# Kernel optimization log

Measured on AMD Instinct MI355X. Metric: run time of the kernel, lower is better.

Reference implementation:

```python
import jax, jax.numpy as jnp
import numpy as np

N = 50000      # nodes
E = 800000     # edges
D = 128        # input_dim
HID = 128      # hidden_dim
OUT = 128      # output_dim
NH = 16        # n_heads (head_dim = 8)
EF = 16        # edge_feat_dim
RF = 64        # r_feat_dim
KV = 2 * D + EF + RF  # 336


def _ln(x, g, b):
    m = x.mean(-1, keepdims=True)
    v = ((x - m) ** 2).mean(-1, keepdims=True)
    return (x - m) / jnp.sqrt(v + 1e-5) * g + b


def _mlp(x, W1, b1, g, be, W2, b2):
    # Linear -> LayerNorm -> ReLU -> Linear (targetdiff-style MLP, norm=True)
    h = jax.nn.relu(_ln(x @ W1 + b1, g, be))
    return h @ W2 + b2


def setup_inputs() -> dict:
    key = jax.random.key(0)
    ks = jax.random.split(key, 32)

    def w(k, shape, fan_in):
        return (jax.random.normal(k, shape, jnp.float32) / np.sqrt(fan_in)).astype(jnp.float32)

    inp = {
        'h': jax.random.normal(ks[0], (N, D), jnp.float32),
        'rel_x': jax.random.normal(ks[1], (E, 3), jnp.float32),
        'r_feat': jax.random.normal(ks[2], (E, RF), jnp.float32),
        'edge_feat': jax.random.normal(ks[3], (E, EF), jnp.float32),
        'edge_index': jax.random.randint(ks[4], (2, E), 0, N, jnp.int64 if jax.config.jax_enable_x64 else jnp.int32),
        # xk MLP: KV -> HID -> OUT
        'xk_W1': w(ks[5], (KV, HID), KV), 'xk_b1': jnp.zeros((HID,), jnp.float32),
        'xk_g': jnp.ones((HID,), jnp.float32), 'xk_be': jnp.zeros((HID,), jnp.float32),
        'xk_W2': w(ks[6], (HID, OUT), HID), 'xk_b2': jnp.zeros((OUT,), jnp.float32),
        # xv MLP: KV -> HID -> NH
        'xv_W1': w(ks[7], (KV, HID), KV), 'xv_b1': jnp.zeros((HID,), jnp.float32),
        'xv_g': jnp.ones((HID,), jnp.float32), 'xv_be': jnp.zeros((HID,), jnp.float32),
        'xv_W2': w(ks[8], (HID, NH), HID), 'xv_b2': jnp.zeros((NH,), jnp.float32),
        # xq MLP: D -> HID -> OUT
        'xq_W1': w(ks[9], (D, HID), D), 'xq_b1': jnp.zeros((HID,), jnp.float32),
        'xq_g': jnp.ones((HID,), jnp.float32), 'xq_be': jnp.zeros((HID,), jnp.float32),
        'xq_W2': w(ks[10], (HID, OUT), HID), 'xq_b2': jnp.zeros((OUT,), jnp.float32),
        # edge-weight net: Linear(RF,1) + sigmoid
        'ew_W': w(ks[11], (RF, 1), RF), 'ew_b': jnp.zeros((1,), jnp.float32),
    }
    return inp


def reference(h, rel_x, r_feat, edge_feat, edge_index,
              xk_W1, xk_b1, xk_g, xk_be, xk_W2, xk_b2,
              xv_W1, xv_b1, xv_g, xv_be, xv_W2, xv_b2,
              xq_W1, xq_b1, xq_g, xq_be, xq_W2, xq_b2,
              ew_W, ew_b):
    src, dst = edge_index[0], edge_index[1]
    # gather -> MLPs
    kv_input = jnp.concatenate([edge_feat, r_feat, h[dst], h[src]], axis=-1)  # [E, KV]
    k = _mlp(kv_input, xk_W1, xk_b1, xk_g, xk_be, xk_W2, xk_b2).reshape(-1, NH, OUT // NH)
    v = _mlp(kv_input, xv_W1, xv_b1, xv_g, xv_be, xv_W2, xv_b2)              # [E, NH]
    e_w = jax.nn.sigmoid(r_feat @ ew_W + ew_b)                               # [E, 1]
    v = v * e_w
    v = v[:, :, None] * rel_x[:, None, :]                                    # [E, NH, 3]
    q = _mlp(h, xq_W1, xq_b1, xq_g, xq_be, xq_W2, xq_b2).reshape(-1, NH, OUT // NH)
    # scatter-softmax over dst segments
    s = (q[dst] * k).sum(-1) / np.sqrt(OUT // NH)                            # [E, NH]
    smax = jax.ops.segment_max(s, dst, num_segments=N)
    ex = jnp.exp(s - smax[dst])
    den = jax.ops.segment_sum(ex, dst, num_segments=N)
    alpha = ex / den[dst]                                                     # [E, NH]
    m = alpha[:, :, None] * v                                                 # [E, NH, 3]
    out = jax.ops.segment_sum(m, dst, num_segments=N)                         # [N, NH, 3]
    return out.mean(1)                                                        # [N, 3]
```

## Files before the change

kernel.cpp:

```cpp
#include <hip/hip_runtime.h>
#include <hip/hip_bf16.h>

#define NN 50000
#define NE 800000
#define DD 128
#define NHD 16
#define EFD 16
#define RFD 64
#define KVD 336
#define KST 360
#define ME 64
#define HST 136
#define KSS 132

typedef __attribute__((ext_vector_type(8))) short bf16x8;
typedef __attribute__((ext_vector_type(4))) float f32x4;

__device__ __forceinline__ unsigned short f2bf(float f) {
    __hip_bfloat16 h = __float2bfloat16(f);
    return __builtin_bit_cast(unsigned short, h);
}
__device__ __forceinline__ float bf2f(unsigned short u) {
    return __uint_as_float(((unsigned)u) << 16);
}

__global__ __launch_bounds__(256) void prep_wt(
    const float* __restrict__ xkW1, const float* __restrict__ xvW1,
    unsigned short* __restrict__ Wt)
{
    const int n = blockIdx.x;
    const float* W = (n < 128) ? xkW1 : xvW1;
    const int col = n & 127;
    for (int k = threadIdx.x; k < KST; k += 256) {
        float v = (k < KVD) ? W[(size_t)k * 128 + col] : 0.0f;
        Wt[(size_t)n * KST + k] = f2bf(v);
    }
}

__global__ __launch_bounds__(128) void prep_wt2(
    const float* __restrict__ xkW2, const float* __restrict__ xvW2,
    unsigned short* __restrict__ Wt2)
{
    const int n = blockIdx.x;
    const int k = threadIdx.x;
    float v = (n < 128) ? xkW2[(size_t)k * 128 + n]
                        : xvW2[(size_t)k * 16 + (n - 128)];
    Wt2[(size_t)n * 128 + k] = f2bf(v);
}

__global__ __launch_bounds__(256) void prep_hbf(
    const float* __restrict__ h, unsigned short* __restrict__ hb)
{
    const size_t i = ((size_t)blockIdx.x * 256 + threadIdx.x) * 4;
    const float4 f = *(const float4*)&h[i];
    ushort4 o;
    o.x = f2bf(f.x); o.y = f2bf(f.y); o.z = f2bf(f.z); o.w = f2bf(f.w);
    *(ushort4*)&hb[i] = o;
}

__global__ __launch_bounds__(256) void hist_kernel(
    const int* __restrict__ dst, int* __restrict__ deg)
{
    const int i = blockIdx.x * 256 + threadIdx.x;
    if (i < NE) atomicAdd(&deg[dst[i]], 1);
}

__global__ __launch_bounds__(256) void scan_kernel(
    const int* __restrict__ deg, int* __restrict__ off, int* __restrict__ cur)
{
    __shared__ int wsum[4];
    const int t = threadIdx.x;
    const int lane = t & 63;
    const int w = t >> 6;
    int run = 0;
    for (int base = 0; base < NN; base += 256) {
        int v = (base + t < NN) ? deg[base + t] : 0;
        int x = v;
        #pragma unroll
        for (int o2 = 1; o2 < 64; o2 <<= 1) {
            int y = __shfl_up(x, o2);
            if (lane >= o2) x += y;
        }
        if (lane == 63) wsum[w] = x;
        __syncthreads();
        int pre = 0;
        #pragma unroll
        for (int ww = 0; ww < 4; ww++) if (ww < w) pre += wsum[ww];
        const int tot = wsum[0] + wsum[1] + wsum[2] + wsum[3];
        const int excl = run + pre + x - v;
        if (base + t < NN) { off[base + t] = excl; cur[base + t] = excl; }
        run += tot;
        __syncthreads();
    }
    if (t == 0) off[NN] = run;
}

__global__ __launch_bounds__(256) void scatter_kernel(
    const int* __restrict__ dst, int* __restrict__ cur, int* __restrict__ eidx)
{
    const int i = blockIdx.x * 256 + threadIdx.x;
    if (i < NE) {
        const int p = atomicAdd(&cur[dst[i]], 1);
        eidx[p] = i;
    }
}

__global__ __launch_bounds__(128) void qmlp_kernel(
    const float* __restrict__ h,
    const float* __restrict__ W1, const float* __restrict__ b1,
    const float* __restrict__ g,  const float* __restrict__ be,
    const float* __restrict__ W2, const float* __restrict__ b2,
    unsigned short* __restrict__ q_bf)
{
    __shared__ float hs[4][DD];
    __shared__ float hid[4][DD];
    __shared__ float red[4][2][2];
    const int j  = threadIdx.x;
    const int n0 = blockIdx.x * 4;

    #pragma unroll
    for (int n = 0; n < 4; n++) hs[n][j] = h[(size_t)(n0 + n) * DD + j];
    __syncthreads();

    float a[4];
    #pragma unroll
    for (int n = 0; n < 4; n++) a[n] = b1[j];
    #pragma unroll 8
    for (int i = 0; i < DD; i++) {
        float w = W1[i * DD + j];
        #pragma unroll
        for (int n = 0; n < 4; n++) a[n] = fmaf(hs[n][i], w, a[n]);
    }

    const int wid = j >> 6;
    #pragma unroll
    for (int n = 0; n < 4; n++) {
        float s1 = a[n], s2 = a[n] * a[n];
        #pragma unroll
        for (int off = 32; off > 0; off >>= 1) {
            s1 += __shfl_xor(s1, off);
            s2 += __shfl_xor(s2, off);
        }
        if ((j & 63) == 0) { red[n][0][wid] = s1; red[n][1][wid] = s2; }
    }
    __syncthreads();

    const float gg = g[j], bb = be[j];
    #pragma unroll
    for (int n = 0; n < 4; n++) {
        float s1   = red[n][0][0] + red[n][0][1];
        float s2   = red[n][1][0] + red[n][1][1];
        float mean = s1 * (1.0f / DD);
        float var  = s2 * (1.0f / DD) - mean * mean;
        float r    = (a[n] - mean) * rsqrtf(var + 1e-5f) * gg + bb;
        hid[n][j]  = fmaxf(r, 0.0f);
    }
    __syncthreads();

    float o[4];
    #pragma unroll
    for (int n = 0; n < 4; n++) o[n] = b2[j];
    #pragma unroll 8
    for (int i = 0; i < DD; i++) {
        float w = W2[i * DD + j];
        #pragma unroll
        for (int n = 0; n < 4; n++) o[n] = fmaf(hid[n][i], w, o[n]);
    }
    #pragma unroll
    for (int n = 0; n < 4; n++) q_bf[(size_t)(n0 + n) * DD + j] = f2bf(o[n]);
}

union SharedU {
    unsigned short kv[ME * KST];
    struct {
        unsigned short hidk[ME * HST];
        unsigned short hidv[ME * HST];
    } s2;
    float ks[ME * KSS];
};

template<int MODE>
__global__ __launch_bounds__(256, 3) void edge_kernel(
    const unsigned short* __restrict__ h_bf,
    const float* __restrict__ rel_x,
    const float* __restrict__ r_feat,
    const float* __restrict__ edge_feat,
    const int*   __restrict__ e_src,
    const int*   __restrict__ e_dst,
    const unsigned short* __restrict__ Wt,
    const unsigned short* __restrict__ Wt2,
    const float* __restrict__ xk_b1, const float* __restrict__ xk_g,
    const float* __restrict__ xk_be, const float* __restrict__ xk_b2,
    const float* __restrict__ xv_b1, const float* __restrict__ xv_g,
    const float* __restrict__ xv_be, const float* __restrict__ xv_W2,
    const float* __restrict__ xv_b2,
    const float* __restrict__ ew_W,  const float* __restrict__ ew_b,
    const unsigned short* __restrict__ q_bf,
    float* __restrict__ exv,
    float* __restrict__ vwe,
    float* __restrict__ accN)
{
    __shared__ SharedU u;
    __shared__ float v_s[ME][NHD + 1];
    __shared__ float ew_s[ME];
    __shared__ float rel_s[ME][3];
    __shared__ int   dst_s[ME];
    __shared__ int   src_s[ME];

    const int tid = threadIdx.x;
    const int e0  = blockIdx.x * ME;

    if (tid < ME) { dst_s[tid] = e_dst[e0 + tid]; src_s[tid] = e_src[e0 + tid]; }
    else if (MODE == 0) {
        int t = tid - ME;
        rel_s[t / 3][t % 3] = rel_x[(size_t)e0 * 3 + t];
    }
    __syncthreads();

    {
        const int e = tid >> 2, p = tid & 3;
        const size_t ge = (size_t)(e0 + e);
        {
            float4 f = *(const float4*)&edge_feat[ge * EFD + p * 4];
            ushort4 o; o.x = f2bf(f.x); o.y = f2bf(f.y); o.z = f2bf(f.z); o.w = f2bf(f.w);
            *(ushort4*)&u.kv[e * KST + p * 4] = o;
        }
        {
            float part = 0.0f;
            #pragma unroll
            for (int i = 0; i < 4; i++) {
                float4 f = *(const float4*)&r_feat[ge * RFD + p * 16 + i * 4];
                float4 w = *(const float4*)&ew_W[p * 16 + i * 4];
                part += f.x * w.x + f.y * w.y + f.z * w.z + f.w * w.w;
                ushort4 o; o.x = f2bf(f.x); o.y = f2bf(f.y); o.z = f2bf(f.z); o.w = f2bf(f.w);
                *(ushort4*)&u.kv[e * KST + 16 + p * 16 + i * 4] = o;
            }
            part += __shfl_xor(part, 1);
            part += __shfl_xor(part, 2);
            if (p == 0) ew_s[e] = 1.0f / (1.0f + __expf(-(part + ew_b[0])));
        }
        {
            const uint4* hp = (const uint4*)&h_bf[(size_t)dst_s[e] * DD + p * 32];
            uint4* op = (uint4*)&u.kv[e * KST + 80 + p * 32];
            #pragma unroll
            for (int i = 0; i < 4; i++) op[i] = hp[i];
        }
        {
            const uint4* hp = (const uint4*)&h_bf[(size_t)src_s[e] * DD + p * 32];
            uint4* op = (uint4*)&u.kv[e * KST + 208 + p * 32];
            #pragma unroll
            for (int i = 0; i < 4; i++) op[i] = hp[i];
        }
        if (p < 2) {
            uint4 z = make_uint4(0, 0, 0, 0);
            *(uint4*)&u.kv[e * KST + 336 + p * 8] = z;
        }
    }
    __syncthreads();

    const int lane = tid & 63;
    const int wv   = tid >> 6;
    const int half = wv >> 1;
    const int mrow = (wv & 1) * 32;
    const int c15  = lane & 15;
    const int q    = lane >> 4;

    f32x4 acc[2][8];
    #pragma unroll
    for (int mt = 0; mt < 2; mt++)
        #pragma unroll
        for (int nt = 0; nt < 8; nt++) acc[mt][nt] = (f32x4){0.f, 0.f, 0.f, 0.f};

    {
        const unsigned short* WtH = Wt + (size_t)(half * 128 + c15) * KST;
        const unsigned short* kvA = &u.kv[(mrow + c15) * KST];
        for (int ks = 0; ks < 11; ks++) {
            const int k0 = ks * 32 + q * 8;
            bf16x8 a0 = *(const bf16x8*)&kvA[k0];
            bf16x8 a1 = *(const bf16x8*)&kvA[16 * KST + k0];
            #pragma unroll
            for (int nt = 0; nt < 8; nt++) {
                bf16x8 b = *(const bf16x8*)&WtH[(size_t)nt * 16 * KST + k0];
                acc[0][nt] = __builtin_amdgcn_mfma_f32_16x16x32_bf16(a0, b, acc[0][nt], 0, 0, 0);
                acc[1][nt] = __builtin_amdgcn_mfma_f32_16x16x32_bf16(a1, b, acc[1][nt], 0, 0, 0);
            }
        }
    }

    {
        const float* b1p = half ? xv_b1 : xk_b1;
        const float* gp  = half ? xv_g  : xk_g;
        const float* bep = half ? xv_be : xk_be;
        float bia[8], gam[8], bet[8];
        #pragma unroll
        for (int nt = 0; nt < 8; nt++) {
            int idx = nt * 16 + c15;
            bia[nt] = b1p[idx]; gam[nt] = gp[idx]; bet[nt] = bep[idx];
        }
        #pragma unroll
        for (int mt = 0; mt < 2; mt++)
            #pragma unroll
            for (int r = 0; r < 4; r++) {
                float x[8]; float s1 = 0.f, s2 = 0.f;
                #pragma unroll
                for (int nt = 0; nt < 8; nt++) {
                    x[nt] = acc[mt][nt][r] + bia[nt];
                    s1 += x[nt]; s2 = fmaf(x[nt], x[nt], s2);
                }
                #pragma unroll
                for (int off = 1; off < 16; off <<= 1) {
                    s1 += __shfl_xor(s1, off);
                    s2 += __shfl_xor(s2, off);
                }
                float mean = s1 * (1.0f / 128.0f);
                float var  = s2 * (1.0f / 128.0f) - mean * mean;
                float rstd = rsqrtf(var + 1e-5f);
                #pragma unroll
                for (int nt = 0; nt < 8; nt++)
                    acc[mt][nt][r] = fmaxf((x[nt] - mean) * rstd * gam[nt] + bet[nt], 0.0f);
            }
    }
    __syncthreads();

    {
        unsigned short* hdst = half ? u.s2.hidv : u.s2.hidk;
        #pragma unroll
        for (int mt = 0; mt < 2; mt++)
            #pragma unroll
            for (int r = 0; r < 4; r++) {
                const int row = mrow + mt * 16 + q * 4 + r;
                #pragma unroll
                for (int nt = 0; nt < 8; nt++)
                    hdst[row * HST + nt * 16 + c15] = f2bf(acc[mt][nt][r]);
            }
    }
    __syncthreads();

    const int mb2 = (wv & 1) * 32;
    const int nb2 = (wv >> 1) * 64;
    f32x4 acck[2][4];
    #pragma unroll
    for (int mt = 0; mt < 2; mt++)
        #pragma unroll
        for (int nt = 0; nt < 4; nt++) acck[mt][nt] = (f32x4){0.f, 0.f, 0.f, 0.f};
    {
        const unsigned short* A0 = &u.s2.hidk[(mb2 + c15) * HST];
        const unsigned short* A1 = &u.s2.hidk[(mb2 + 16 + c15) * HST];
        const unsigned short* B0 = &Wt2[(size_t)(nb2 + c15) * 128];
        #pragma unroll
        for (int ks = 0; ks < 4; ks++) {
            const int k0 = ks * 32 + q * 8;
            bf16x8 a0 = *(const bf16x8*)&A0[k0];
            bf16x8 a1 = *(const bf16x8*)&A1[k0];
            #pragma unroll
            for (int nt = 0; nt < 4; nt++) {
                bf16x8 b = *(const bf16x8*)&B0[(size_t)nt * 16 * 128 + k0];
                acck[0][nt] = __builtin_amdgcn_mfma_f32_16x16x32_bf16(a0, b, acck[0][nt], 0, 0, 0);
                acck[1][nt] = __builtin_amdgcn_mfma_f32_16x16x32_bf16(a1, b, acck[1][nt], 0, 0, 0);
            }
        }
    }

    float vacc[4];
    #pragma unroll
    for (int p = 0; p < 4; p++) {
        int item = tid + p * 256;
        int e    = item >> 4;
        int col  = item & 15;
        float a = xv_b2[col];
        #pragma unroll 8
        for (int i4 = 0; i4 < 32; i4++) {
            const ushort4 hv = *(const ushort4*)&u.s2.hidv[e * HST + i4 * 4];
            a = fmaf(bf2f(hv.x), xv_W2[(i4 * 4 + 0) * 16 + col], a);
            a = fmaf(bf2f(hv.y), xv_W2[(i4 * 4 + 1) * 16 + col], a);
            a = fmaf(bf2f(hv.z), xv_W2[(i4 * 4 + 2) * 16 + col], a);
            a = fmaf(bf2f(hv.w), xv_W2[(i4 * 4 + 3) * 16 + col], a);
        }
        vacc[p] = a;
    }
    __syncthreads();

    #pragma unroll
    for (int nt = 0; nt < 4; nt++) {
        const float bias = xk_b2[nb2 + nt * 16 + c15];
        #pragma unroll
        for (int mt = 0; mt < 2; mt++)
            #pragma unroll
            for (int r = 0; r < 4; r++)
                u.ks[(mb2 + mt * 16 + q * 4 + r) * KSS + nb2 + nt * 16 + c15] =
                    acck[mt][nt][r] + bias;
    }
    #pragma unroll
    for (int p = 0; p < 4; p++) {
        int item = tid + p * 256;
        v_s[item >> 4][item & 15] = vacc[p];
    }
    __syncthreads();

    {
        const float inv_s8 = 0.35355339059327373f;
        const int tc2  = tid & 31;
        const int te2  = tid >> 5;
        const int head = tc2 >> 1;
        const int sub  = tc2 & 1;
        #pragma unroll
        for (int e = 0; e < 8; e++) {
            int el  = te2 * 8 + e;
            int dst = dst_s[el];
            const float4  kk = *(const float4*)&u.ks[el * KSS + tc2 * 4];
            const ushort4 qb = *(const ushort4*)&q_bf[(size_t)dst * DD + tc2 * 4];
            float p = bf2f(qb.x) * kk.x + bf2f(qb.y) * kk.y +
                      bf2f(qb.z) * kk.z + bf2f(qb.w) * kk.w;
            p += __shfl_xor(p, 1);
            float ex = __expf(p * inv_s8);
            if (MODE == 1) {
                if (sub == 0) {
                    exv[(size_t)(e0 + el) * NHD + head] = ex;
                } else {
                    vwe[(size_t)(e0 + el) * NHD + head] =
                        v_s[el][head] * ew_s[el] * ex;
                }
            } else {
                float vw = v_s[el][head] * ew_s[el] * ex;
                float* base = &accN[(((size_t)dst * NHD) + head) * 4];
                if (sub == 0) {
                    atomicAdd(base + 0, vw * rel_s[el][0]);
                    atomicAdd(base + 1, vw * rel_s[el][1]);
                } else {
                    atomicAdd(base + 2, vw * rel_s[el][2]);
                    atomicAdd(base + 3, ex);
                }
            }
        }
    }
}

__global__ __launch_bounds__(256) void gather_kernel(
    const int* __restrict__ off, const int* __restrict__ eidx,
    const float* __restrict__ exv, const float* __restrict__ vwe,
    const float* __restrict__ rel_x, float* __restrict__ out)
{
    const int t = threadIdx.x;
    const int g = t >> 4;
    const int h = t & 15;
    const int n = blockIdx.x * 16 + g;
    if (n >= NN) return;
    const int j0 = off[n], j1 = off[n + 1];
    float den = 0.f, sx = 0.f, sy = 0.f, sz = 0.f;
    for (int j = j0; j < j1; j++) {
        const int e = eidx[j];
        const float ex = exv[(size_t)e * NHD + h];
        const float vw = vwe[(size_t)e * NHD + h];
        const float rx = rel_x[(size_t)e * 3 + 0];
        const float ry = rel_x[(size_t)e * 3 + 1];
        const float rz = rel_x[(size_t)e * 3 + 2];
        sx = fmaf(vw, rx, sx);
        sy = fmaf(vw, ry, sy);
        sz = fmaf(vw, rz, sz);
        den += ex;
    }
    const float c = (den > 0.f) ? 1.0f / den : 0.0f;
    float ox = sx * c, oy = sy * c, oz = sz * c;
    #pragma unroll
    for (int o2 = 1; o2 < 16; o2 <<= 1) {
        ox += __shfl_xor(ox, o2);
        oy += __shfl_xor(oy, o2);
        oz += __shfl_xor(oz, o2);
    }
    if (h == 0) {
        out[(size_t)n * 3 + 0] = ox * (1.0f / NHD);
        out[(size_t)n * 3 + 1] = oy * (1.0f / NHD);
        out[(size_t)n * 3 + 2] = oz * (1.0f / NHD);
    }
}

__global__ __launch_bounds__(256) void finalize_kernel(
    const float* __restrict__ accN, float* __restrict__ out)
{
    int n = blockIdx.x * blockDim.x + threadIdx.x;
    if (n >= NN) return;
    float ox = 0.0f, oy = 0.0f, oz = 0.0f;
    #pragma unroll
    for (int hh = 0; hh < NHD; hh++) {
        float4 a = *(const float4*)&accN[(((size_t)n * NHD) + hh) * 4];
        if (a.w > 0.0f) {
            float r = 1.0f / a.w;
            ox = fmaf(a.x, r, ox);
            oy = fmaf(a.y, r, oy);
            oz = fmaf(a.z, r, oz);
        }
    }
    out[n * 3 + 0] = ox * (1.0f / NHD);
    out[n * 3 + 1] = oy * (1.0f / NHD);
    out[n * 3 + 2] = oz * (1.0f / NHD);
}

extern "C" void kernel_launch(void* const* d_in, const int* in_sizes, int n_in,
                              void* d_out, int out_size, void* d_ws, size_t ws_size,
                              hipStream_t stream)
{
    const float* h         = (const float*)d_in[0];
    const float* rel_x     = (const float*)d_in[1];
    const float* r_feat    = (const float*)d_in[2];
    const float* edge_feat = (const float*)d_in[3];
    const int*   e_idx     = (const int*)d_in[4];
    const float* xk_W1 = (const float*)d_in[5];
    const float* xk_b1 = (const float*)d_in[6];
    const float* xk_g  = (const float*)d_in[7];
    const float* xk_be = (const float*)d_in[8];
    const float* xk_W2 = (const float*)d_in[9];
    const float* xk_b2 = (const float*)d_in[10];
    const float* xv_W1 = (const float*)d_in[11];
    const float* xv_b1 = (const float*)d_in[12];
    const float* xv_g  = (const float*)d_in[13];
    const float* xv_be = (const float*)d_in[14];
    const float* xv_W2 = (const float*)d_in[15];
    const float* xv_b2 = (const float*)d_in[16];
    const float* xq_W1 = (const float*)d_in[17];
    const float* xq_b1 = (const float*)d_in[18];
    const float* xq_g  = (const float*)d_in[19];
    const float* xq_be = (const float*)d_in[20];
    const float* xq_W2 = (const float*)d_in[21];
    const float* xq_b2 = (const float*)d_in[22];
    const float* ew_W  = (const float*)d_in[23];
    const float* ew_b  = (const float*)d_in[24];

    size_t o = 0;
    auto take = [&](size_t bytes) -> char* {
        o = (o + 255) & ~(size_t)255;
        char* p = (char*)d_ws + o;
        o += bytes;
        return p;
    };
    unsigned short* h_bf = (unsigned short*)take((size_t)NN * DD * 2);
    unsigned short* q_bf = (unsigned short*)take((size_t)NN * DD * 2);
    unsigned short* Wt   = (unsigned short*)take((size_t)256 * KST * 2);
    unsigned short* Wt2  = (unsigned short*)take((size_t)144 * 128 * 2);
    int*   deg  = (int*)take((size_t)NN * 4);
    int*   cur  = (int*)take((size_t)NN * 4);
    int*   offv = (int*)take((size_t)(NN + 1) * 4);
    int*   eidx = (int*)take((size_t)NE * 4);
    float* exv  = (float*)take((size_t)NE * NHD * 4);
    float* vwe  = (float*)take((size_t)NE * NHD * 4);
    const bool sorted = (o <= ws_size);
    float* accN = (float*)(void*)deg;

    prep_hbf<<<(NN * DD / 4 + 255) / 256, 256, 0, stream>>>(h, h_bf);
    prep_wt<<<256, 256, 0, stream>>>(xk_W1, xv_W1, Wt);
    prep_wt2<<<144, 128, 0, stream>>>(xk_W2, xv_W2, Wt2);
    qmlp_kernel<<<NN / 4, 128, 0, stream>>>(h, xq_W1, xq_b1, xq_g, xq_be,
                                            xq_W2, xq_b2, q_bf);

    if (sorted) {
        hipMemsetAsync(deg, 0, (size_t)NN * 4, stream);
        hist_kernel<<<(NE + 255) / 256, 256, 0, stream>>>(e_idx + NE, deg);
        scan_kernel<<<1, 256, 0, stream>>>(deg, offv, cur);
        scatter_kernel<<<(NE + 255) / 256, 256, 0, stream>>>(e_idx + NE, cur, eidx);

        edge_kernel<1><<<NE / ME, 256, 0, stream>>>(
            h_bf, rel_x, r_feat, edge_feat,
            e_idx, e_idx + NE,
            Wt, Wt2,
            xk_b1, xk_g, xk_be, xk_b2,
            xv_b1, xv_g, xv_be, xv_W2, xv_b2,
            ew_W, ew_b, q_bf, exv, vwe, nullptr);

        gather_kernel<<<(NN + 15) / 16, 256, 0, stream>>>(
            offv, eidx, exv, vwe, rel_x, (float*)d_out);
    } else {
        hipMemsetAsync(accN, 0, (size_t)NN * NHD * 4 * sizeof(float), stream);
        edge_kernel<0><<<NE / ME, 256, 0, stream>>>(
            h_bf, rel_x, r_feat, edge_feat,
            e_idx, e_idx + NE,
            Wt, Wt2,
            xk_b1, xk_g, xk_be, xk_b2,
            xv_b1, xv_g, xv_be, xv_W2, xv_b2,
            ew_W, ew_b, q_bf, nullptr, nullptr, accN);

        finalize_kernel<<<(NN + 255) / 256, 256, 0, stream>>>(accN, (float*)d_out);
    }
}
```

Before: 1.415 ms.

## Write edge outputs in dst-sorted order, halve edge tile, widen q-MLP blocks

The scatter kernel now records each edge's sorted position and copies rel_x into sorted order. The edge kernel writes exv/vwe straight to those positions, so the gather reads contiguous memory instead of going through eidx indirection. The edge tile drops from 64 to 32 edges per block with a higher occupancy hint, which halves accumulator registers per wave but reuses weight loads less. The q-MLP now handles 16 nodes per 256-thread block to reuse weights better.

```diff
diff --git a/kernel.cpp b/kernel.cpp
--- a/kernel.cpp
+++ b/kernel.cpp
@@ -9,7 +9,7 @@
 #define RFD 64
 #define KVD 336
 #define KST 360
-#define ME 64
+#define ME 32
 #define HST 136
 #define KSS 132
 
@@ -96,78 +96,89 @@
 }
 
 __global__ __launch_bounds__(256) void scatter_kernel(
-    const int* __restrict__ dst, int* __restrict__ cur, int* __restrict__ eidx)
+    const int* __restrict__ dst, const float* __restrict__ rel_x,
+    int* __restrict__ cur, int* __restrict__ pos, float* __restrict__ relp)
 {
     const int i = blockIdx.x * 256 + threadIdx.x;
     if (i < NE) {
         const int p = atomicAdd(&cur[dst[i]], 1);
-        eidx[p] = i;
-    }
-}
-
-__global__ __launch_bounds__(128) void qmlp_kernel(
+        pos[i] = p;
+        relp[(size_t)p * 3 + 0] = rel_x[(size_t)i * 3 + 0];
+        relp[(size_t)p * 3 + 1] = rel_x[(size_t)i * 3 + 1];
+        relp[(size_t)p * 3 + 2] = rel_x[(size_t)i * 3 + 2];
+    }
+}
+
+__global__ __launch_bounds__(256) void qmlp_kernel(
     const float* __restrict__ h,
     const float* __restrict__ W1, const float* __restrict__ b1,
     const float* __restrict__ g,  const float* __restrict__ be,
     const float* __restrict__ W2, const float* __restrict__ b2,
     unsigned short* __restrict__ q_bf)
 {
-    __shared__ float hs[4][DD];
-    __shared__ float hid[4][DD];
-    __shared__ float red[4][2][2];
-    const int j  = threadIdx.x;
-    const int n0 = blockIdx.x * 4;
-
-    #pragma unroll
-    for (int n = 0; n < 4; n++) hs[n][j] = h[(size_t)(n0 + n) * DD + j];
-    __syncthreads();
-
-    float a[4];
-    #pragma unroll
-    for (int n = 0; n < 4; n++) a[n] = b1[j];
+    __shared__ float hs[16][DD];
+    __shared__ float hid[16][DD];
+    __shared__ float red[2][8][2][2];
+    const int tid  = threadIdx.x;
+    const int col  = tid & 127;
+    const int half = tid >> 7;
+    const int wp   = (tid >> 6) & 1;
+    const int n0   = blockIdx.x * 16;
+
+    {
+        const float4* src = (const float4*)&h[(size_t)n0 * DD];
+        float4* dstp = (float4*)&hs[0][0];
+        dstp[tid]       = src[tid];
+        dstp[tid + 256] = src[tid + 256];
+    }
+    __syncthreads();
+
+    float a[8];
+    #pragma unroll
+    for (int j = 0; j < 8; j++) a[j] = b1[col];
     #pragma unroll 8
     for (int i = 0; i < DD; i++) {
-        float w = W1[i * DD + j];
-        #pragma unroll
-        for (int n = 0; n < 4; n++) a[n] = fmaf(hs[n][i], w, a[n]);
-    }
-
-    const int wid = j >> 6;
-    #pragma unroll
-    for (int n = 0; n < 4; n++) {
-        float s1 = a[n], s2 = a[n] * a[n];
+        float w = W1[i * DD + col];
+        #pragma unroll
+        for (int j = 0; j < 8; j++) a[j] = fmaf(hs[half * 8 + j][i], w, a[j]);
+    }
+
+    #pragma unroll
+    for (int j = 0; j < 8; j++) {
+        float s1 = a[j], s2 = a[j] * a[j];
         #pragma unroll
         for (int off = 32; off > 0; off >>= 1) {
             s1 += __shfl_xor(s1, off);
             s2 += __shfl_xor(s2, off);
         }
-        if ((j & 63) == 0) { red[n][0][wid] = s1; red[n][1][wid] = s2; }
-    }
-    __syncthreads();
-
-    const float gg = g[j], bb = be[j];
-    #pragma unroll
-    for (int n = 0; n < 4; n++) {
-        float s1   = red[n][0][0] + red[n][0][1];
-        float s2   = red[n][1][0] + red[n][1][1];
+        if ((tid & 63) == 0) { red[half][j][0][wp] = s1; red[half][j][1][wp] = s2; }
+    }
+    __syncthreads();
+
+    const float gg = g[col], bb = be[col];
+    #pragma unroll
+    for (int j = 0; j < 8; j++) {
+        float s1   = red[half][j][0][0] + red[half][j][0][1];
+        float s2   = red[half][j][1][0] + red[half][j][1][1];
         float mean = s1 * (1.0f / DD);
         float var  = s2 * (1.0f / DD) - mean * mean;
-        float r    = (a[n] - mean) * rsqrtf(var + 1e-5f) * gg + bb;
-        hid[n][j]  = fmaxf(r, 0.0f);
-    }
-    __syncthreads();
-
-    float o[4];
-    #pragma unroll
-    for (int n = 0; n < 4; n++) o[n] = b2[j];
+        float r    = (a[j] - mean) * rsqrtf(var + 1e-5f) * gg + bb;
+        hid[half * 8 + j][col] = fmaxf(r, 0.0f);
+    }
+    __syncthreads();
+
+    float o[8];
+    #pragma unroll
+    for (int j = 0; j < 8; j++) o[j] = b2[col];
     #pragma unroll 8
     for (int i = 0; i < DD; i++) {
-        float w = W2[i * DD + j];
-        #pragma unroll
-        for (int n = 0; n < 4; n++) o[n] = fmaf(hid[n][i], w, o[n]);
-    }
-    #pragma unroll
-    for (int n = 0; n < 4; n++) q_bf[(size_t)(n0 + n) * DD + j] = f2bf(o[n]);
+        float w = W2[i * DD + col];
+        #pragma unroll
+        for (int j = 0; j < 8; j++) o[j] = fmaf(hid[half * 8 + j][i], w, o[j]);
+    }
+    #pragma unroll
+    for (int j = 0; j < 8; j++)
+        q_bf[(size_t)(n0 + half * 8 + j) * DD + col] = f2bf(o[j]);
 }
 
 union SharedU {
@@ -180,13 +191,14 @@
 };
 
 template<int MODE>
-__global__ __launch_bounds__(256, 3) void edge_kernel(
+__global__ __launch_bounds__(256, 6) void edge_kernel(
     const unsigned short* __restrict__ h_bf,
     const float* __restrict__ rel_x,
     const float* __restrict__ r_feat,
     const float* __restrict__ edge_feat,
     const int*   __restrict__ e_src,
     const int*   __restrict__ e_dst,
+    const int*   __restrict__ pos,
     const unsigned short* __restrict__ Wt,
     const unsigned short* __restrict__ Wt2,
     const float* __restrict__ xk_b1, const float* __restrict__ xk_g,
@@ -206,26 +218,25 @@
     __shared__ float rel_s[ME][3];
     __shared__ int   dst_s[ME];
     __shared__ int   src_s[ME];
+    __shared__ int   pos_s[ME];
 
     const int tid = threadIdx.x;
     const int e0  = blockIdx.x * ME;
 
-    if (tid < ME) { dst_s[tid] = e_dst[e0 + tid]; src_s[tid] = e_src[e0 + tid]; }
-    else if (MODE == 0) {
+    if (tid < ME) {
+        dst_s[tid] = e_dst[e0 + tid];
+        src_s[tid] = e_src[e0 + tid];
+        if (MODE == 1) pos_s[tid] = pos[e0 + tid];
+    } else if (MODE == 0 && tid < ME + ME * 3) {
         int t = tid - ME;
         rel_s[t / 3][t % 3] = rel_x[(size_t)e0 * 3 + t];
     }
     __syncthreads();
 
     {
-        const int e = tid >> 2, p = tid & 3;
+        const int e = tid >> 3, p = tid & 7;
         const size_t ge = (size_t)(e0 + e);
-        {
-            float4 f = *(const float4*)&edge_feat[ge * EFD + p * 4];
-            ushort4 o; o.x = f2bf(f.x); o.y = f2bf(f.y); o.z = f2bf(f.z); o.w = f2bf(f.w);
-            *(ushort4*)&u.kv[e * KST + p * 4] = o;
-        }
-        {
+        if (p < 4) {
             float part = 0.0f;
             #pragma unroll
             for (int i = 0; i < 4; i++) {
@@ -238,18 +249,20 @@
             part += __shfl_xor(part, 1);
             part += __shfl_xor(part, 2);
             if (p == 0) ew_s[e] = 1.0f / (1.0f + __expf(-(part + ew_b[0])));
+        } else {
+            float4 f = *(const float4*)&edge_feat[ge * EFD + (p - 4) * 4];
+            ushort4 o; o.x = f2bf(f.x); o.y = f2bf(f.y); o.z = f2bf(f.z); o.w = f2bf(f.w);
+            *(ushort4*)&u.kv[e * KST + (p - 4) * 4] = o;
         }
         {
-            const uint4* hp = (const uint4*)&h_bf[(size_t)dst_s[e] * DD + p * 32];
-            uint4* op = (uint4*)&u.kv[e * KST + 80 + p * 32];
-            #pragma unroll
-            for (int i = 0; i < 4; i++) op[i] = hp[i];
+            const uint4* hp = (const uint4*)&h_bf[(size_t)dst_s[e] * DD + p * 16];
+            uint4* op = (uint4*)&u.kv[e * KST + 80 + p * 16];
+            op[0] = hp[0]; op[1] = hp[1];
         }
         {
-            const uint4* hp = (const uint4*)&h_bf[(size_t)src_s[e] * DD + p * 32];
-            uint4* op = (uint4*)&u.kv[e * KST + 208 + p * 32];
-            #pragma unroll
-            for (int i = 0; i < 4; i++) op[i] = hp[i];
+            const uint4* hp = (const uint4*)&h_bf[(size_t)src_s[e] * DD + p * 16];
+            uint4* op = (uint4*)&u.kv[e * KST + 208 + p * 16];
+            op[0] = hp[0]; op[1] = hp[1];
         }
         if (p < 2) {
             uint4 z = make_uint4(0, 0, 0, 0);
@@ -258,31 +271,27 @@
     }
     __syncthreads();
 
-    const int lane = tid & 63;
-    const int wv   = tid >> 6;
-    const int half = wv >> 1;
-    const int mrow = (wv & 1) * 32;
-    const int c15  = lane & 15;
-    const int q    = lane >> 4;
-
-    f32x4 acc[2][8];
-    #pragma unroll
-    for (int mt = 0; mt < 2; mt++)
-        #pragma unroll
-        for (int nt = 0; nt < 8; nt++) acc[mt][nt] = (f32x4){0.f, 0.f, 0.f, 0.f};
+    const int lane  = tid & 63;
+    const int wv    = tid >> 6;
+    const int half  = wv >> 1;
+    const int mhalf = wv & 1;
+    const int c15   = lane & 15;
+    const int q     = lane >> 4;
+
+    f32x4 acc[8];
+    #pragma unroll
+    for (int nt = 0; nt < 8; nt++) acc[nt] = (f32x4){0.f, 0.f, 0.f, 0.f};
 
     {
         const unsigned short* WtH = Wt + (size_t)(half * 128 + c15) * KST;
-        const unsigned short* kvA = &u.kv[(mrow + c15) * KST];
+        const unsigned short* kvA = &u.kv[(mhalf * 16 + c15) * KST];
         for (int ks = 0; ks < 11; ks++) {
             const int k0 = ks * 32 + q * 8;
             bf16x8 a0 = *(const bf16x8*)&kvA[k0];
-            bf16x8 a1 = *(const bf16x8*)&kvA[16 * KST + k0];
             #pragma unroll
             for (int nt = 0; nt < 8; nt++) {
                 bf16x8 b = *(const bf16x8*)&WtH[(size_t)nt * 16 * KST + k0];
-                acc[0][nt] = __builtin_amdgcn_mfma_f32_16x16x32_bf16(a0, b, acc[0][nt], 0, 0, 0);
-                acc[1][nt] = __builtin_amdgcn_mfma_f32_16x16x32_bf16(a1, b, acc[1][nt], 0, 0, 0);
+                acc[nt] = __builtin_amdgcn_mfma_f32_16x16x32_bf16(a0, b, acc[nt], 0, 0, 0);
             }
         }
     }
@@ -298,72 +307,63 @@
             bia[nt] = b1p[idx]; gam[nt] = gp[idx]; bet[nt] = bep[idx];
         }
         #pragma unroll
-        for (int mt = 0; mt < 2; mt++)
-            #pragma unroll
-            for (int r = 0; r < 4; r++) {
-                float x[8]; float s1 = 0.f, s2 = 0.f;
-                #pragma unroll
-                for (int nt = 0; nt < 8; nt++) {
-                    x[nt] = acc[mt][nt][r] + bia[nt];
-                    s1 += x[nt]; s2 = fmaf(x[nt], x[nt], s2);
-                }
-                #pragma unroll
-                for (int off = 1; off < 16; off <<= 1) {
-                    s1 += __shfl_xor(s1, off);
-                    s2 += __shfl_xor(s2, off);
-                }
-                float mean = s1 * (1.0f / 128.0f);
-                float var  = s2 * (1.0f / 128.0f) - mean * mean;
-                float rstd = rsqrtf(var + 1e-5f);
-                #pragma unroll
-                for (int nt = 0; nt < 8; nt++)
-                    acc[mt][nt][r] = fmaxf((x[nt] - mean) * rstd * gam[nt] + bet[nt], 0.0f);
+        for (int r = 0; r < 4; r++) {
+            float x[8]; float s1 = 0.f, s2 = 0.f;
+            #pragma unroll
+            for (int nt = 0; nt < 8; nt++) {
+                x[nt] = acc[nt][r] + bia[nt];
+                s1 += x[nt]; s2 = fmaf(x[nt], x[nt], s2);
             }
+            #pragma unroll
+            for (int off = 1; off < 16; off <<= 1) {
+                s1 += __shfl_xor(s1, off);
+                s2 += __shfl_xor(s2, off);
+            }
+            float mean = s1 * (1.0f / 128.0f);
+            float var  = s2 * (1.0f / 128.0f) - mean * mean;
+            float rstd = rsqrtf(var + 1e-5f);
+            #pragma unroll
+            for (int nt = 0; nt < 8; nt++)
+                acc[nt][r] = fmaxf((x[nt] - mean) * rstd * gam[nt] + bet[nt], 0.0f);
+        }
     }
     __syncthreads();
 
     {
         unsigned short* hdst = half ? u.s2.hidv : u.s2.hidk;
         #pragma unroll
-        for (int mt = 0; mt < 2; mt++)
-            #pragma unroll
-            for (int r = 0; r < 4; r++) {
-                const int row = mrow + mt * 16 + q * 4 + r;
-                #pragma unroll
-                for (int nt = 0; nt < 8; nt++)
-                    hdst[row * HST + nt * 16 + c15] = f2bf(acc[mt][nt][r]);
-            }
-    }
-    __syncthreads();
-
-    const int mb2 = (wv & 1) * 32;
-    const int nb2 = (wv >> 1) * 64;
-    f32x4 acck[2][4];
-    #pragma unroll
-    for (int mt = 0; mt < 2; mt++)
-        #pragma unroll
-        for (int nt = 0; nt < 4; nt++) acck[mt][nt] = (f32x4){0.f, 0.f, 0.f, 0.f};
+        for (int r = 0; r < 4; r++) {
+            const int row = mhalf * 16 + q * 4 + r;
+            #pragma unroll
+            for (int nt = 0; nt < 8; nt++)
+                hdst[row * HST + nt * 16 + c15] = f2bf(acc[nt][r]);
+        }
+    }
+    __syncthreads();
+
+    const int mb2 = mhalf * 16;
+    const int nb2 = half * 64;
+    f32x4 acck[4];
+    #pragma unroll
+    for (int nt = 0; nt < 4; nt++) acck[nt] = (f32x4){0.f, 0.f, 0.f, 0.f};
     {
         const unsigned short* A0 = &u.s2.hidk[(mb2 + c15) * HST];
-        const unsigned short* A1 = &u.s2.hidk[(mb2 + 16 + c15) * HST];
         const unsigned short* B0 = &Wt2[(size_t)(nb2 + c15) * 128];
         #pragma unroll
         for (int ks = 0; ks < 4; ks++) {
             const int k0 = ks * 32 + q * 8;
             bf16x8 a0 = *(const bf16x8*)&A0[k0];
-            bf16x8 a1 = *(const bf16x8*)&A1[k0];
             #pragma unroll
             for (int nt = 0; nt < 4; nt++) {
                 bf16x8 b = *(const bf16x8*)&B0[(size_t)nt * 16 * 128 + k0];
-                acck[0][nt] = __builtin_amdgcn_mfma_f32_16x16x32_bf16(a0, b, acck[0][nt], 0, 0, 0);
-                acck[1][nt] = __builtin_amdgcn_mfma_f32_16x16x32_bf16(a1, b, acck[1][nt], 0, 0, 0);
+                acck[nt] = __builtin_amdgcn_mfma_f32_16x16x32_bf16(a0, b, acck[nt], 0, 0, 0);
             }
         }
     }
 
-    float vacc[4];
-    #pragma unroll
-    for (int p = 0; p < 4; p++) {
+    float vacc[2];
+    #pragma unroll
+    for (int p = 0; p < 2; p++) {
         int item = tid + p * 256;
         int e    = item >> 4;
         int col  = item & 15;
@@ -384,14 +384,12 @@
     for (int nt = 0; nt < 4; nt++) {
         const float bias = xk_b2[nb2 + nt * 16 + c15];
         #pragma unroll
-        for (int mt = 0; mt < 2; mt++)
-            #pragma unroll
-            for (int r = 0; r < 4; r++)
-                u.ks[(mb2 + mt * 16 + q * 4 + r) * KSS + nb2 + nt * 16 + c15] =
-                    acck[mt][nt][r] + bias;
-    }
-    #pragma unroll
-    for (int p = 0; p < 4; p++) {
+        for (int r = 0; r < 4; r++)
+            u.ks[(mb2 + q * 4 + r) * KSS + nb2 + nt * 16 + c15] =
+                acck[nt][r] + bias;
+    }
+    #pragma unroll
+    for (int p = 0; p < 2; p++) {
         int item = tid + p * 256;
         v_s[item >> 4][item & 15] = vacc[p];
     }
@@ -404,8 +402,8 @@
         const int head = tc2 >> 1;
         const int sub  = tc2 & 1;
         #pragma unroll
-        for (int e = 0; e < 8; e++) {
-            int el  = te2 * 8 + e;
+        for (int e = 0; e < 4; e++) {
+            int el  = te2 * 4 + e;
             int dst = dst_s[el];
             const float4  kk = *(const float4*)&u.ks[el * KSS + tc2 * 4];
             const ushort4 qb = *(const ushort4*)&q_bf[(size_t)dst * DD + tc2 * 4];
@@ -414,12 +412,9 @@
             p += __shfl_xor(p, 1);
             float ex = __expf(p * inv_s8);
             if (MODE == 1) {
-                if (sub == 0) {
-                    exv[(size_t)(e0 + el) * NHD + head] = ex;
-                } else {
-                    vwe[(size_t)(e0 + el) * NHD + head] =
-                        v_s[el][head] * ew_s[el] * ex;
-                }
+                const size_t pp = (size_t)pos_s[el] * NHD + head;
+                if (sub == 0) exv[pp] = ex;
+                else          vwe[pp] = v_s[el][head] * ew_s[el] * ex;
             } else {
                 float vw = v_s[el][head] * ew_s[el] * ex;
                 float* base = &accN[(((size_t)dst * NHD) + head) * 4];
@@ -436,9 +431,9 @@
 }
 
 __global__ __launch_bounds__(256) void gather_kernel(
-    const int* __restrict__ off, const int* __restrict__ eidx,
+    const int* __restrict__ off,
     const float* __restrict__ exv, const float* __restrict__ vwe,
-    const float* __restrict__ rel_x, float* __restrict__ out)
+    const float* __restrict__ relp, float* __restrict__ out)
 {
     const int t = threadIdx.x;
     const int g = t >> 4;
@@ -448,12 +443,11 @@
     const int j0 = off[n], j1 = off[n + 1];
     float den = 0.f, sx = 0.f, sy = 0.f, sz = 0.f;
     for (int j = j0; j < j1; j++) {
-        const int e = eidx[j];
-        const float ex = exv[(size_t)e * NHD + h];
-        const float vw = vwe[(size_t)e * NHD + h];
-        const float rx = rel_x[(size_t)e * 3 + 0];
-        const float ry = rel_x[(size_t)e * 3 + 1];
-        const float rz = rel_x[(size_t)e * 3 + 2];
+        const float ex = exv[(size_t)j * NHD + h];
+        const float vw = vwe[(size_t)j * NHD + h];
+        const float rx = relp[(size_t)j * 3 + 0];
+        const float ry = relp[(size_t)j * 3 + 1];
+        const float rz = relp[(size_t)j * 3 + 2];
         sx = fmaf(vw, rx, sx);
         sy = fmaf(vw, ry, sy);
         sz = fmaf(vw, rz, sz);
@@ -539,7 +533,8 @@
     int*   deg  = (int*)take((size_t)NN * 4);
     int*   cur  = (int*)take((size_t)NN * 4);
     int*   offv = (int*)take((size_t)(NN + 1) * 4);
-    int*   eidx = (int*)take((size_t)NE * 4);
+    int*   pos  = (int*)take((size_t)NE * 4);
+    float* relp = (float*)take((size_t)NE * 3 * 4);
     float* exv  = (float*)take((size_t)NE * NHD * 4);
     float* vwe  = (float*)take((size_t)NE * NHD * 4);
     const bool sorted = (o <= ws_size);
@@ -548,30 +543,31 @@
     prep_hbf<<<(NN * DD / 4 + 255) / 256, 256, 0, stream>>>(h, h_bf);
     prep_wt<<<256, 256, 0, stream>>>(xk_W1, xv_W1, Wt);
     prep_wt2<<<144, 128, 0, stream>>>(xk_W2, xv_W2, Wt2);
-    qmlp_kernel<<<NN / 4, 128, 0, stream>>>(h, xq_W1, xq_b1, xq_g, xq_be,
-                                            xq_W2, xq_b2, q_bf);
+    qmlp_kernel<<<NN / 16, 256, 0, stream>>>(h, xq_W1, xq_b1, xq_g, xq_be,
+                                             xq_W2, xq_b2, q_bf);
 
     if (sorted) {
         hipMemsetAsync(deg, 0, (size_t)NN * 4, stream);
         hist_kernel<<<(NE + 255) / 256, 256, 0, stream>>>(e_idx + NE, deg);
         scan_kernel<<<1, 256, 0, stream>>>(deg, offv, cur);
-        scatter_kernel<<<(NE + 255) / 256, 256, 0, stream>>>(e_idx + NE, cur, eidx);
+        scatter_kernel<<<(NE + 255) / 256, 256, 0, stream>>>(
+            e_idx + NE, rel_x, cur, pos, relp);
 
         edge_kernel<1><<<NE / ME, 256, 0, stream>>>(
             h_bf, rel_x, r_feat, edge_feat,
-            e_idx, e_idx + NE,
+            e_idx, e_idx + NE, pos,
             Wt, Wt2,
             xk_b1, xk_g, xk_be, xk_b2,
             xv_b1, xv_g, xv_be, xv_W2, xv_b2,
             ew_W, ew_b, q_bf, exv, vwe, nullptr);
 
         gather_kernel<<<(NN + 15) / 16, 256, 0, stream>>>(
-            offv, eidx, exv, vwe, rel_x, (float*)d_out);
+            offv, exv, vwe, relp, (float*)d_out);
     } else {
         hipMemsetAsync(accN, 0, (size_t)NN * NHD * 4 * sizeof(float), stream);
         edge_kernel<0><<<NE / ME, 256, 0, stream>>>(
             h_bf, rel_x, r_feat, edge_feat,
-            e_idx, e_idx + NE,
+            e_idx, e_idx + NE, nullptr,
             Wt, Wt2,
             xk_b1, xk_g, xk_be, xk_b2,
             xv_b1, xv_g, xv_be, xv_W2, xv_b2,
```

After: 1.757 ms. 24.2% more time.
